# Kernel optimization log

Hardware: AMD Instinct MI355X
Metric: run time of the kernel (lower is better)

## Reference

```python
import jax, jax.numpy as jnp
import numpy as np

B, T, E = 2, 2048, 2048
H = 16
DH = E // H  # 128
FFN = 4 * E  # 8192
EPS = 1e-5


def _layernorm(x, g, b):
    mu = jnp.mean(x, axis=-1, keepdims=True)
    var = jnp.mean((x - mu) ** 2, axis=-1, keepdims=True)
    return (x - mu) * jax.lax.rsqrt(var + EPS) * g + b


def setup_inputs() -> dict:
    key = jax.random.key(0)
    ks = jax.random.split(key, 8)
    s = 0.02
    return {
        "x": jax.random.normal(ks[0], (B, T, E), jnp.float32),
        "g1": jnp.ones((E,), jnp.float32),
        "b1": jnp.zeros((E,), jnp.float32),
        "wq": jax.random.normal(ks[1], (E, E), jnp.float32) * s,
        "wk": jax.random.normal(ks[2], (E, E), jnp.float32) * s,
        "wv": jax.random.normal(ks[3], (E, E), jnp.float32) * s,
        "wo": jax.random.normal(ks[4], (E, E), jnp.float32) * s,
        "g2": jnp.ones((E,), jnp.float32),
        "b2": jnp.zeros((E,), jnp.float32),
        "w1": jax.random.normal(ks[5], (E, FFN), jnp.float32) * s,
        "w2": jax.random.normal(ks[6], (E, FFN), jnp.float32) * s,
        "w3": jax.random.normal(ks[7], (FFN, E), jnp.float32) * s,
    }


def reference(x, g1, b1, wq, wk, wv, wo, g2, b2, w1, w2, w3):
    Bx, Tx, Ex = x.shape
    # --- attention block (pre-LN, residual) ---
    h = _layernorm(x, g1, b1)
    q = (h @ wq).reshape(Bx, Tx, H, DH)
    k = (h @ wk).reshape(Bx, Tx, H, DH)
    v = (h @ wv).reshape(Bx, Tx, H, DH)
    scores = jnp.einsum('bqhd,bkhd->bhqk', q, k) / jnp.sqrt(jnp.float32(DH))
    causal = jnp.tril(jnp.ones((Tx, Tx), bool))  # [T,T]
    scores = jnp.where(causal[None, None], scores, -jnp.inf)
    attn = jax.nn.softmax(scores, axis=-1)
    ctx = jnp.einsum('bhqk,bkhd->bqhd', attn, v).reshape(Bx, Tx, H * DH)
    x = x + ctx @ wo
    # --- SwiGLU MLP block (pre-LN, residual) ---
    h = _layernorm(x, g2, b2)
    gated = jax.nn.silu(h @ w1) * (h @ w2)
    return x + gated @ w3
```

## Files before the change

kernel.cpp:

```cpp
#include <hip/hip_runtime.h>


#define T_SEQ 2048
#define E_DIM 2048
#define N_HEAD 16
#define D_HEAD 128
#define FFN_DIM 8192
#define M_ROWS 4096
#define QS (3 * E_DIM)

typedef unsigned short u16;
typedef short short8 __attribute__((ext_vector_type(8)));
typedef float f32x4 __attribute__((ext_vector_type(4)));

#define DEV __device__ __forceinline__

DEV u16 f2bf(float f) {
  unsigned u = __float_as_uint(f);
  u += 0x7fffu + ((u >> 16) & 1u);
  return (u16)(u >> 16);
}
DEV float bf2f(u16 h) { return __uint_as_float(((unsigned)h) << 16); }

DEV void async16(void* lds, const void* g) {
  __builtin_amdgcn_global_load_lds((const __attribute__((address_space(1))) void*)g,
                                   (__attribute__((address_space(3))) void*)lds, 16, 0, 0);
}

__global__ __launch_bounds__(256) void ln_kernel(const float* __restrict__ x,
                                                 const float* __restrict__ gw,
                                                 const float* __restrict__ bw,
                                                 u16* __restrict__ out) {
  int row = blockIdx.x;
  int t = threadIdx.x;
  const float4* xr = (const float4*)(x + (size_t)row * E_DIM);
  float4 a = xr[t], c = xr[t + 256];
  float s = a.x + a.y + a.z + a.w + c.x + c.y + c.z + c.w;
  float q = a.x * a.x + a.y * a.y + a.z * a.z + a.w * a.w +
            c.x * c.x + c.y * c.y + c.z * c.z + c.w * c.w;
  for (int off = 32; off > 0; off >>= 1) {
    s += __shfl_down(s, off);
    q += __shfl_down(q, off);
  }
  __shared__ float red[8];
  if ((t & 63) == 0) { red[(t >> 6) * 2] = s; red[(t >> 6) * 2 + 1] = q; }
  __syncthreads();
  s = red[0] + red[2] + red[4] + red[6];
  q = red[1] + red[3] + red[5] + red[7];
  float mu = s * (1.f / E_DIM);
  float rs = rsqrtf(q * (1.f / E_DIM) - mu * mu + 1e-5f);
  const float4* g4 = (const float4*)gw;
  const float4* b4 = (const float4*)bw;
  float4 g0 = g4[t], g1v = g4[t + 256], e0 = b4[t], e1 = b4[t + 256];
  ushort4 o0, o1;
  o0.x = f2bf((a.x - mu) * rs * g0.x + e0.x);
  o0.y = f2bf((a.y - mu) * rs * g0.y + e0.y);
  o0.z = f2bf((a.z - mu) * rs * g0.z + e0.z);
  o0.w = f2bf((a.w - mu) * rs * g0.w + e0.w);
  o1.x = f2bf((c.x - mu) * rs * g1v.x + e1.x);
  o1.y = f2bf((c.y - mu) * rs * g1v.y + e1.y);
  o1.z = f2bf((c.z - mu) * rs * g1v.z + e1.z);
  o1.w = f2bf((c.w - mu) * rs * g1v.w + e1.w);
  ((ushort4*)(out + (size_t)row * E_DIM))[t] = o0;
  ((ushort4*)(out + (size_t)row * E_DIM))[t + 256] = o1;
}

__global__ __launch_bounds__(256) void cvt_t_kernel(const float* __restrict__ W,
                                                    u16* __restrict__ WT,
                                                    int Kd, int Nd) {
  __shared__ float tile[32][33];
  int tx = threadIdx.x, ty = threadIdx.y;
  int n0 = blockIdx.x * 32, k0 = blockIdx.y * 32;
#pragma unroll
  for (int i = 0; i < 4; i++)
    tile[ty + i * 8][tx] = W[(size_t)(k0 + ty + i * 8) * Nd + n0 + tx];
  __syncthreads();
#pragma unroll
  for (int i = 0; i < 4; i++)
    WT[(size_t)(n0 + ty + i * 8) * Kd + k0 + tx] = f2bf(tile[tx][ty + i * 8]);
}

__global__ __launch_bounds__(256) void transpose_v_kernel(const u16* __restrict__ qkv,
                                                          u16* __restrict__ vt) {
  __shared__ u16 tile[32][33];
  int tx = threadIdx.x, ty = threadIdx.y;
  int b = blockIdx.z;
  int t0 = blockIdx.x * 32, e0 = blockIdx.y * 32;
#pragma unroll
  for (int i = 0; i < 4; i++)
    tile[ty + i * 8][tx] =
        qkv[(size_t)(b * T_SEQ + t0 + ty + i * 8) * QS + 2 * E_DIM + e0 + tx];
  __syncthreads();
#pragma unroll
  for (int i = 0; i < 4; i++)
    vt[((size_t)b * E_DIM + e0 + ty + i * 8) * T_SEQ + t0 + tx] = tile[tx][ty + i * 8];
}

__global__ __launch_bounds__(256) void add3_kernel(float* __restrict__ out,
                                                   const u16* __restrict__ pk) {
  const size_t MN = (size_t)M_ROWS * E_DIM;
  size_t base = ((size_t)blockIdx.x * 256 + threadIdx.x) * 8;
  short8 a = *(const short8*)(pk + base);
  short8 b = *(const short8*)(pk + MN + base);
  float4 o0 = *(float4*)(out + base), o1 = *(float4*)(out + base + 4);
  o0.x += bf2f((u16)a[0]) + bf2f((u16)b[0]);
  o0.y += bf2f((u16)a[1]) + bf2f((u16)b[1]);
  o0.z += bf2f((u16)a[2]) + bf2f((u16)b[2]);
  o0.w += bf2f((u16)a[3]) + bf2f((u16)b[3]);
  o1.x += bf2f((u16)a[4]) + bf2f((u16)b[4]);
  o1.y += bf2f((u16)a[5]) + bf2f((u16)b[5]);
  o1.z += bf2f((u16)a[6]) + bf2f((u16)b[6]);
  o1.w += bf2f((u16)a[7]) + bf2f((u16)b[7]);
  *(float4*)(out + base) = o0;
  *(float4*)(out + base + 4) = o1;
}

template <int MODE, int BM_>
__global__ __launch_bounds__(512, 1) void gemm8p(const u16* __restrict__ A,
                                                 const u16* __restrict__ BT,
                                                 void* __restrict__ Cout,
                                                 const void* __restrict__ Extra,
                                                 int N, int K, int lda, int ldb,
                                                 int CX, int CY) {
  constexpr int MM = BM_ / 64;
  constexpr int AUNIT = BM_ * 32;
  __shared__ u16 Abuf[4 * AUNIT];
  __shared__ u16 Bbuf[4 * 8192];
  const int t = threadIdx.x;
  const int w = t >> 6, l = t & 63, g = l >> 4, lq = l & 15;
  const int wm = w >> 2, wn = w & 3;

  const int bid = (blockIdx.z * gridDim.y + blockIdx.y) * gridDim.x + blockIdx.x;
  const int xcd = bid & 7, slot = bid >> 3;
  const int nchx = gridDim.x / CX;
  const int nchy = gridDim.y / CY;
  const int cpz = nchx * nchy;
  const int kz = xcd / cpz;
  const int cid = xcd % cpz;
  const int bx = (cid % nchx) * CX + (slot % CX);
  const int by = (cid / nchx) * CY + (slot / CX);
  const size_t bm = (size_t)by * BM_, bn = (size_t)bx * 256;
  const size_t koff = (size_t)kz * K;

  const int srcrow = ((l >> 3) << 1) | (l & 1);
  const int csrc = ((((l >> 1) & 3) ^ ((l >> 3) & 3)) << 3);
  const u16* aSrc = A + (bm + w * 16 + srcrow) * (size_t)lda + koff + csrc;
  const u16* bSrc = BT + (bn + w * 16 + srcrow) * (size_t)ldb + koff + csrc;
  const int rdoff = (((lq & 1) + 2 * (g ^ ((lq >> 1) & 3))) << 3);

#define STA8(DB, KS, TILE)                                                    \
  {                                                                           \
    u16* Ad = Abuf + (DB) * (2 * AUNIT) + (KS)*AUNIT + w * 512;               \
    const u16* as_ = aSrc + (size_t)(TILE)*64 + (KS)*32;                      \
    async16(Ad, as_);                                                         \
    if constexpr (BM_ == 256) async16(Ad + 4096, as_ + (size_t)128 * lda);    \
  }
#define STB8(DB, KS, TILE)                                                    \
  {                                                                           \
    u16* Bd = Bbuf + (DB)*16384 + (KS)*8192 + w * 512;                        \
    const u16* bs_ = bSrc + (size_t)(TILE)*64 + (KS)*32;                      \
    async16(Bd, bs_);                                                         \
    async16(Bd + 4096, bs_ + (size_t)128 * ldb);                              \
  }
#define RDA8(DB, KS, MH)                                                      \
  _Pragma("unroll") for (int mm = 0; mm < MM; ++mm)                           \
      af[mm] = *(const short8*)(Abuf + (DB) * (2 * AUNIT) + (KS)*AUNIT +      \
                                (wm * (BM_ / 4) + (MH) * (BM_ / 8) + mm * 8 + \
                                 (lq >> 1)) * 64 + rdoff);
#define RDB8(DB, KS)                                                          \
  _Pragma("unroll") for (int nn = 0; nn < 4; ++nn)                            \
      bf[nn] = *(const short8*)(Bbuf + (DB)*16384 + (KS)*8192 +               \
                                (wn * 32 + nn * 8 + (lq >> 1)) * 64 + rdoff);
#define MM168(MH)                                                             \
  _Pragma("unroll") for (int mm = 0; mm < MM; ++mm)                           \
      _Pragma("unroll") for (int nn = 0; nn < 4; ++nn)                        \
          acc[(MH)*MM + mm][nn] = __builtin_amdgcn_mfma_f32_16x16x32_bf16(    \
              af[mm], bf[nn], acc[(MH)*MM + mm][nn], 0, 0, 0);
#define SYNCA                                                                 \
  __builtin_amdgcn_s_barrier();                                               \
  asm volatile("s_waitcnt lgkmcnt(0)" ::: "memory");                          \
  __builtin_amdgcn_sched_barrier(0);                                          \
  __builtin_amdgcn_s_setprio(1);
#define ENDP __builtin_amdgcn_s_setprio(0);
#define BAR2 __builtin_amdgcn_s_barrier();
#define WAITN                                                                 \
  if constexpr (BM_ == 256) asm volatile("s_waitcnt vmcnt(8)" ::: "memory");  \
  else                      asm volatile("s_waitcnt vmcnt(6)" ::: "memory");
#define WAITH                                                                 \
  if constexpr (BM_ == 256) asm volatile("s_waitcnt vmcnt(4)" ::: "memory");  \
  else                      asm volatile("s_waitcnt vmcnt(3)" ::: "memory");

  const int NT = K >> 6, NI = NT >> 1;
  f32x4 acc[2 * MM][4] = {};
  short8 af[MM > 4 ? MM : 4], bf[4];

  STA8(0, 0, 0); STB8(0, 0, 0);
  STA8(0, 1, 0); STB8(0, 1, 0);
  STA8(1, 0, 1); STB8(1, 0, 1);
  WAITN;
  BAR2;

  for (int j = 0; j < NI; ++j) {
    const int t1 = 2 * j + 1, t2 = 2 * j + 2, t3 = 2 * j + 3;
    const bool s2 = t2 < NT, s3 = t3 < NT, lastI = (j + 1 == NI);
    RDB8(0, 0); RDA8(0, 0, 0);
    STA8(1, 1, t1);
    SYNCA; MM168(0); ENDP; BAR2;
    RDA8(0, 0, 1);
    STB8(1, 1, t1);
    SYNCA; MM168(1); ENDP;
    WAITN;
    BAR2;
    RDB8(0, 1); RDA8(0, 1, 0);
    if (s2) STA8(0, 0, t2);
    SYNCA; MM168(0); ENDP; BAR2;
    RDA8(0, 1, 1);
    if (s2) STB8(0, 0, t2);
    SYNCA; MM168(1); ENDP;
    if (lastI) { WAITH; } else { WAITN; }
    BAR2;
    RDB8(1, 0); RDA8(1, 0, 0);
    if (s2) STA8(0, 1, t2);
    SYNCA; MM168(0); ENDP; BAR2;
    RDA8(1, 0, 1);
    if (s2) STB8(0, 1, t2);
    SYNCA; MM168(1); ENDP;
    if (lastI) { asm volatile("s_waitcnt vmcnt(0)" ::: "memory"); } else { WAITN; }
    BAR2;
    RDB8(1, 1); RDA8(1, 1, 0);
    if (s3) STA8(1, 0, t3);
    SYNCA; MM168(0); ENDP; BAR2;
    RDA8(1, 1, 1);
    if (s3) STB8(1, 0, t3);
    SYNCA; MM168(1); ENDP;
    if (!lastI) { WAITN; }
    BAR2;
  }
#undef STA8
#undef STB8
#undef RDA8
#undef RDB8
#undef MM168
#undef SYNCA
#undef ENDP
#undef BAR2
#undef WAITN
#undef WAITH

  const size_t mn = (size_t)gridDim.y * BM_ * (size_t)N;
#pragma unroll
  for (int m = 0; m < 2 * MM; m++) {
    size_t row = bm + wm * (BM_ / 2) + m * 16 + 4 * g;
#pragma unroll
    for (int n = 0; n < 4; n++) {
      size_t col = bn + wn * 64 + n * 16 + lq;
#pragma unroll
      for (int r = 0; r < 4; r++) {
        size_t idx = (row + r) * (size_t)N + col;
        if constexpr (MODE == 0) {
          ((u16*)Cout)[idx] = f2bf(acc[m][n][r]);
        } else if constexpr (MODE == 1) {
          ((float*)Cout)[idx] = ((const float*)Extra)[idx] + acc[m][n][r];
        } else if constexpr (MODE == 2) {
          float a = bf2f(((const u16*)Extra)[idx]);
          float sil = a / (1.f + exp2f(-1.4426950408889634f * a));
          ((u16*)Cout)[idx] = f2bf(sil * acc[m][n][r]);
        } else {
          ((u16*)Cout)[(size_t)kz * mn + idx] = f2bf(acc[m][n][r]);
        }
      }
    }
  }
}

__global__ __launch_bounds__(256, 2) void attn_kernel(const u16* __restrict__ QKV,
                                                      const u16* __restrict__ VT,
                                                      u16* __restrict__ CTX) {
  __shared__ u16 Ks[64 * 128];
  __shared__ u16 Vs[128 * 64];
  __shared__ u16 P_all[4][32 * 72];
  const int t = threadIdx.x;
  const int w = t >> 6, l = t & 63, g = l >> 4, lq = l & 15;
  u16* P = P_all[w];
  const int q0blk = blockIdx.x * 128;
  const int q0w = q0blk + w * 32;
  const int bh = blockIdx.y, b = bh >> 4, h = bh & 15;
  const u16* qp = QKV + (size_t)b * T_SEQ * QS + h * D_HEAD;
  const u16* kp = QKV + (size_t)b * T_SEQ * QS + E_DIM + h * D_HEAD;
  const u16* vp = VT + ((size_t)b * E_DIM + h * D_HEAD) * T_SEQ;

  short8 qf[2][4];
#pragma unroll
  for (int rg = 0; rg < 2; rg++)
#pragma unroll
    for (int ks = 0; ks < 4; ks++)
      qf[rg][ks] =
          *(const short8*)(qp + (size_t)(q0w + rg * 16 + lq) * QS + ks * 32 + g * 8);

  f32x4 acc[2][8] = {};
  float m2[2][4], ls[2][4];
#pragma unroll
  for (int rg = 0; rg < 2; rg++)
#pragma unroll
    for (int r = 0; r < 4; r++) { m2[rg][r] = -1e30f; ls[rg][r] = 0.f; }
  const float sc = 0.08838834764831845f * 1.4426950408889634f;

  const int kRow0 = 16 * w + (l >> 4);
  const int kChunk = l & 15;
  const int vRow0 = 32 * w + (l >> 3);
  const int vChunk = l & 7;

  for (int kv0 = 0; kv0 < q0blk + 128; kv0 += 64) {
#pragma unroll
    for (int j = 0; j < 4; j++) {
      int R = kRow0 + 4 * j;
      async16(Ks + (16 * w + 4 * j) * 128,
              kp + (size_t)(kv0 + R) * QS + ((kChunk ^ (R & 7)) << 3));
    }
#pragma unroll
    for (int j = 0; j < 4; j++) {
      int D = vRow0 + 8 * j;
      async16(Vs + (32 * w + 8 * j) * 64,
              vp + (size_t)D * T_SEQ + kv0 + ((vChunk ^ (D & 7)) << 3));
    }
    __syncthreads();

#pragma unroll
    for (int rg = 0; rg < 2; rg++) {
      const int rb = q0w + rg * 16;
      if (kv0 > rb + 15) continue;
      f32x4 s[4];
      __builtin_amdgcn_s_setprio(1);
#pragma unroll
      for (int ct = 0; ct < 4; ct++) {
        s[ct] = f32x4{0.f, 0.f, 0.f, 0.f};
#pragma unroll
        for (int ks = 0; ks < 4; ks++) {
          short8 kf = *(const short8*)(Ks + (ct * 16 + lq) * 128 +
                                       (((ks * 4 + g) ^ (lq & 7)) << 3));
          s[ct] = __builtin_amdgcn_mfma_f32_16x16x32_bf16(qf[rg][ks], kf, s[ct], 0, 0, 0);
        }
      }
      __builtin_amdgcn_s_setprio(0);
      float sv[4][4];
#pragma unroll
      for (int ct = 0; ct < 4; ct++)
#pragma unroll
        for (int r = 0; r < 4; r++) sv[ct][r] = s[ct][r] * sc;
      if (kv0 + 64 > rb) {
#pragma unroll
        for (int ct = 0; ct < 4; ct++)
#pragma unroll
          for (int r = 0; r < 4; r++)
            if (kv0 + ct * 16 + lq > rb + 4 * g + r) sv[ct][r] = -1e30f;
      }
      float mx[4];
#pragma unroll
      for (int r = 0; r < 4; r++)
        mx[r] = fmaxf(fmaxf(sv[0][r], sv[1][r]), fmaxf(sv[2][r], sv[3][r]));
#pragma unroll
      for (int off = 1; off < 16; off <<= 1)
#pragma unroll
        for (int r = 0; r < 4; r++) mx[r] = fmaxf(mx[r], __shfl_xor(mx[r], off));
#pragma unroll
      for (int r = 0; r < 4; r++) {
        float mn = fmaxf(m2[rg][r], mx[r]);
        float sca = exp2f(m2[rg][r] - mn);
        m2[rg][r] = mn;
        float sum = 0.f;
#pragma unroll
        for (int ct = 0; ct < 4; ct++) {
          float pv = exp2f(sv[ct][r] - mn);
          sum += pv;
          P[(rg * 16 + 4 * g + r) * 72 + ct * 16 + lq] = f2bf(pv);
        }
        ls[rg][r] = ls[rg][r] * sca + sum;
#pragma unroll
        for (int n = 0; n < 8; n++) acc[rg][n][r] *= sca;
      }
      short8 pa[2];
#pragma unroll
      for (int ks2 = 0; ks2 < 2; ks2++)
        pa[ks2] = *(const short8*)(P + (rg * 16 + lq) * 72 + ks2 * 32 + g * 8);
      __builtin_amdgcn_s_setprio(1);
#pragma unroll
      for (int n = 0; n < 8; n++)
#pragma unroll
        for (int ks2 = 0; ks2 < 2; ks2++) {
          short8 vf = *(const short8*)(Vs + (n * 16 + lq) * 64 +
                                       (((ks2 * 4 + g) ^ (lq & 7)) << 3));
          acc[rg][n] = __builtin_amdgcn_mfma_f32_16x16x32_bf16(pa[ks2], vf, acc[rg][n], 0, 0, 0);
        }
      __builtin_amdgcn_s_setprio(0);
    }
    __syncthreads();
  }

#pragma unroll
  for (int rg = 0; rg < 2; rg++) {
#pragma unroll
    for (int off = 1; off < 16; off <<= 1)
#pragma unroll
      for (int r = 0; r < 4; r++) ls[rg][r] += __shfl_xor(ls[rg][r], off);
  }
  u16* cp = CTX + ((size_t)b * T_SEQ + q0w) * E_DIM + h * D_HEAD;
#pragma unroll
  for (int rg = 0; rg < 2; rg++) {
    float inv[4];
#pragma unroll
    for (int r = 0; r < 4; r++) inv[r] = 1.f / ls[rg][r];
#pragma unroll
    for (int n = 0; n < 8; n++)
#pragma unroll
      for (int r = 0; r < 4; r++)
        cp[(size_t)(rg * 16 + 4 * g + r) * E_DIM + n * 16 + lq] =
            f2bf(acc[rg][n][r] * inv[r]);
  }
}

extern "C" void kernel_launch(void* const* d_in, const int* in_sizes, int n_in,
                              void* d_out, int out_size, void* d_ws, size_t ws_size,
                              hipStream_t stream) {
  (void)in_sizes; (void)n_in; (void)out_size; (void)ws_size;
  const float* x  = (const float*)d_in[0];
  const float* g1 = (const float*)d_in[1];
  const float* b1 = (const float*)d_in[2];
  const float* wq = (const float*)d_in[3];
  const float* wk = (const float*)d_in[4];
  const float* wv = (const float*)d_in[5];
  const float* wo = (const float*)d_in[6];
  const float* g2 = (const float*)d_in[7];
  const float* b2 = (const float*)d_in[8];
  const float* w1 = (const float*)d_in[9];
  const float* w2 = (const float*)d_in[10];
  const float* w3 = (const float*)d_in[11];
  float* out = (float*)d_out;

  const size_t EE2 = (size_t)E_DIM * E_DIM * 2;
  const size_t EF2 = (size_t)E_DIM * FFN_DIM * 2;
  const size_t ME2 = (size_t)M_ROWS * E_DIM * 2;
  char* p = (char*)d_ws;
  u16* wqkvT = (u16*)p; p += 3 * EE2;
  u16* woT = (u16*)p; p += EE2;
  u16* w1T = (u16*)p; p += EF2;
  u16* w2T = (u16*)p; p += EF2;
  u16* w3T = (u16*)p; p += EF2;
  u16* Hb  = (u16*)p; p += ME2;
  u16* QKVb = (u16*)p; p += (size_t)M_ROWS * QS * 2;
  u16* VTb = (u16*)p; p += ME2;
  u16* CTXb = (u16*)p; p += ME2;
  u16* U1b = QKVb;
  u16* Pk = wqkvT;

  dim3 blk32(32, 8);
  cvt_t_kernel<<<dim3(E_DIM / 32, E_DIM / 32), blk32, 0, stream>>>(wq, wqkvT, E_DIM, E_DIM);
  cvt_t_kernel<<<dim3(E_DIM / 32, E_DIM / 32), blk32, 0, stream>>>(wk, wqkvT + E_DIM * E_DIM, E_DIM, E_DIM);
  cvt_t_kernel<<<dim3(E_DIM / 32, E_DIM / 32), blk32, 0, stream>>>(wv, wqkvT + 2 * E_DIM * E_DIM, E_DIM, E_DIM);
  cvt_t_kernel<<<dim3(E_DIM / 32, E_DIM / 32), blk32, 0, stream>>>(wo, woT, E_DIM, E_DIM);
  cvt_t_kernel<<<dim3(FFN_DIM / 32, E_DIM / 32), blk32, 0, stream>>>(w1, w1T, E_DIM, FFN_DIM);
  cvt_t_kernel<<<dim3(FFN_DIM / 32, E_DIM / 32), blk32, 0, stream>>>(w2, w2T, E_DIM, FFN_DIM);
  cvt_t_kernel<<<dim3(E_DIM / 32, FFN_DIM / 32), blk32, 0, stream>>>(w3, w3T, FFN_DIM, E_DIM);

  ln_kernel<<<M_ROWS, 256, 0, stream>>>(x, g1, b1, Hb);
  gemm8p<0, 256><<<dim3(QS / 256, M_ROWS / 256), 512, 0, stream>>>(
      Hb, wqkvT, QKVb, nullptr, QS, E_DIM, E_DIM, E_DIM, 6, 8);
  transpose_v_kernel<<<dim3(T_SEQ / 32, E_DIM / 32, 2), blk32, 0, stream>>>(QKVb, VTb);
  attn_kernel<<<dim3(T_SEQ / 128, 2 * N_HEAD), 256, 0, stream>>>(QKVb, VTb, CTXb);
  gemm8p<1, 128><<<dim3(E_DIM / 256, M_ROWS / 128), 512, 0, stream>>>(
      CTXb, woT, out, x, E_DIM, E_DIM, E_DIM, E_DIM, 4, 8);

  ln_kernel<<<M_ROWS, 256, 0, stream>>>(out, g2, b2, Hb);
  gemm8p<0, 256><<<dim3(FFN_DIM / 256, M_ROWS / 256), 512, 0, stream>>>(
      Hb, w1T, U1b, nullptr, FFN_DIM, E_DIM, E_DIM, E_DIM, 8, 8);
  gemm8p<2, 256><<<dim3(FFN_DIM / 256, M_ROWS / 256), 512, 0, stream>>>(
      Hb, w2T, U1b, U1b, FFN_DIM, E_DIM, E_DIM, E_DIM, 8, 8);
  gemm8p<3, 256><<<dim3(E_DIM / 256, M_ROWS / 256, 2), 512, 0, stream>>>(
      U1b, w3T, Pk, nullptr, E_DIM, FFN_DIM / 2, FFN_DIM, FFN_DIM, 4, 8);
  add3_kernel<<<4096, 256, 0, stream>>>(out, Pk);
}
```

Before: 893.3 us.

## Fuse W1 and W2 FFN GEMMs into one dual-B kernel with SiLU epilogue

Replaces the two separate FFN up-projection GEMMs (one writing U1 in bf16, the second reading it back to apply SiLU gating) with a single kernel. Each block loads one A tile and matching 128-column tiles of both w1T and w2T. The two products are combined through LDS in the epilogue, so the silu(u1)*u2 result is written once. This removes one full pass over A and the bf16 round trip of the intermediate U1 buffer. In exchange each block covers a narrower 128-column N tile, adds an LDS exchange step in the epilogue, and keeps the pipelined async-load schedule intact.

```diff
diff --git a/kernel.cpp b/kernel.cpp
--- a/kernel.cpp
+++ b/kernel.cpp
@@ -273,6 +273,166 @@
   }
 }
 
+__global__ __launch_bounds__(512, 1) void gemm_ffn(const u16* __restrict__ A,
+                                                   const u16* __restrict__ B1T,
+                                                   const u16* __restrict__ B2T,
+                                                   u16* __restrict__ Cout,
+                                                   int N, int K, int lda, int ldb,
+                                                   int CX, int CY) {
+  constexpr int AUNIT = 8192;
+  __shared__ u16 Abuf[4 * AUNIT];
+  __shared__ u16 Bbuf[4 * AUNIT];
+  const int t = threadIdx.x;
+  const int w = t >> 6, l = t & 63, g = l >> 4, lq = l & 15;
+  const int wm = w >> 2, wn = w & 3;
+
+  const int bid = blockIdx.y * gridDim.x + blockIdx.x;
+  const int xcd = bid & 7, slot = bid >> 3;
+  const int nchx = gridDim.x / CX;
+  const int cid = xcd;
+  const int bx = (cid % nchx) * CX + (slot % CX);
+  const int by = (cid / nchx) * CY + (slot / CX);
+  const size_t bm = (size_t)by * 256;
+  const size_t c0 = (size_t)bx * 128;
+
+  const int srcrow = ((l >> 3) << 1) | (l & 1);
+  const int csrc = ((((l >> 1) & 3) ^ ((l >> 3) & 3)) << 3);
+  const u16* aSrc = A + (bm + w * 16 + srcrow) * (size_t)lda + csrc;
+  const u16* b1Src = B1T + (c0 + w * 16 + srcrow) * (size_t)ldb + csrc;
+  const u16* b2Src = B2T + (c0 + w * 16 + srcrow) * (size_t)ldb + csrc;
+  const int rdoff = (((lq & 1) + 2 * (g ^ ((lq >> 1) & 3))) << 3);
+
+#define STA8(DB, KS, TILE)                                                    \
+  {                                                                           \
+    u16* Ad = Abuf + (DB) * (2 * AUNIT) + (KS)*AUNIT + w * 512;               \
+    const u16* as_ = aSrc + (size_t)(TILE)*64 + (KS)*32;                      \
+    async16(Ad, as_);                                                         \
+    async16(Ad + 4096, as_ + (size_t)128 * lda);                              \
+  }
+#define STB8(DB, KS, TILE)                                                    \
+  {                                                                           \
+    u16* Bd = Bbuf + (DB) * (2 * AUNIT) + (KS)*AUNIT + w * 512;               \
+    size_t off_ = (size_t)(TILE)*64 + (KS)*32;                                \
+    async16(Bd, b1Src + off_);                                                \
+    async16(Bd + 4096, b2Src + off_);                                         \
+  }
+#define RDA8(DB, KS, MH)                                                      \
+  _Pragma("unroll") for (int mm = 0; mm < 4; ++mm)                            \
+      af[mm] = *(const short8*)(Abuf + (DB) * (2 * AUNIT) + (KS)*AUNIT +      \
+                                (wm * 64 + (MH)*32 + mm * 8 + (lq >> 1)) *    \
+                                    64 + rdoff);
+#define RDB8(DB, KS)                                                          \
+  _Pragma("unroll") for (int nn = 0; nn < 4; ++nn)                            \
+      bf[nn] = *(const short8*)(Bbuf + (DB) * (2 * AUNIT) + (KS)*AUNIT +      \
+                                (wn * 32 + nn * 8 + (lq >> 1)) * 64 + rdoff);
+#define MM168(MH)                                                             \
+  _Pragma("unroll") for (int mm = 0; mm < 4; ++mm)                            \
+      _Pragma("unroll") for (int nn = 0; nn < 4; ++nn)                        \
+          acc[(MH)*4 + mm][nn] = __builtin_amdgcn_mfma_f32_16x16x32_bf16(     \
+              af[mm], bf[nn], acc[(MH)*4 + mm][nn], 0, 0, 0);
+#define SYNCA                                                                 \
+  __builtin_amdgcn_s_barrier();                                               \
+  asm volatile("s_waitcnt lgkmcnt(0)" ::: "memory");                          \
+  __builtin_amdgcn_sched_barrier(0);                                          \
+  __builtin_amdgcn_s_setprio(1);
+#define ENDP __builtin_amdgcn_s_setprio(0);
+#define BAR2 __builtin_amdgcn_s_barrier();
+#define WAITN asm volatile("s_waitcnt vmcnt(8)" ::: "memory");
+#define WAITH asm volatile("s_waitcnt vmcnt(4)" ::: "memory");
+
+  const int NT = K >> 6, NI = NT >> 1;
+  f32x4 acc[8][4] = {};
+  short8 af[4], bf[4];
+
+  STA8(0, 0, 0); STB8(0, 0, 0);
+  STA8(0, 1, 0); STB8(0, 1, 0);
+  STA8(1, 0, 1); STB8(1, 0, 1);
+  WAITN;
+  BAR2;
+
+  for (int j = 0; j < NI; ++j) {
+    const int t1 = 2 * j + 1, t2 = 2 * j + 2, t3 = 2 * j + 3;
+    const bool s2 = t2 < NT, s3 = t3 < NT, lastI = (j + 1 == NI);
+    RDB8(0, 0); RDA8(0, 0, 0);
+    STA8(1, 1, t1);
+    SYNCA; MM168(0); ENDP; BAR2;
+    RDA8(0, 0, 1);
+    STB8(1, 1, t1);
+    SYNCA; MM168(1); ENDP;
+    WAITN;
+    BAR2;
+    RDB8(0, 1); RDA8(0, 1, 0);
+    if (s2) STA8(0, 0, t2);
+    SYNCA; MM168(0); ENDP; BAR2;
+    RDA8(0, 1, 1);
+    if (s2) STB8(0, 0, t2);
+    SYNCA; MM168(1); ENDP;
+    if (lastI) { WAITH; } else { WAITN; }
+    BAR2;
+    RDB8(1, 0); RDA8(1, 0, 0);
+    if (s2) STA8(0, 1, t2);
+    SYNCA; MM168(0); ENDP; BAR2;
+    RDA8(1, 0, 1);
+    if (s2) STB8(0, 1, t2);
+    SYNCA; MM168(1); ENDP;
+    if (lastI) { asm volatile("s_waitcnt vmcnt(0)" ::: "memory"); } else { WAITN; }
+    BAR2;
+    RDB8(1, 1); RDA8(1, 1, 0);
+    if (s3) STA8(1, 0, t3);
+    SYNCA; MM168(0); ENDP; BAR2;
+    RDA8(1, 1, 1);
+    if (s3) STB8(1, 0, t3);
+    SYNCA; MM168(1); ENDP;
+    if (!lastI) { WAITN; }
+    BAR2;
+  }
+#undef STA8
+#undef STB8
+#undef RDA8
+#undef RDB8
+#undef MM168
+#undef SYNCA
+#undef ENDP
+#undef BAR2
+#undef WAITN
+#undef WAITH
+
+  const int reg = wm * 2 + ((wn >= 2) ? (wn - 2) : wn);
+  float* fb = (float*)((reg < 2 ? Abuf : Bbuf) + (reg & 1) * 16384);
+  if (wn >= 2) {
+#pragma unroll
+    for (int m = 0; m < 8; m++)
+#pragma unroll
+      for (int n = 0; n < 4; n++)
+#pragma unroll
+        for (int r = 0; r < 4; r++) {
+          int lrow = m * 16 + 4 * g + r;
+          int pcol = (n * 16 + lq) ^ ((g & 1) << 4);
+          fb[lrow * 64 + pcol] = acc[m][n][r];
+        }
+  }
+  __syncthreads();
+  if (wn < 2) {
+#pragma unroll
+    for (int m = 0; m < 8; m++) {
+      size_t row = bm + wm * 128 + m * 16 + 4 * g;
+#pragma unroll
+      for (int n = 0; n < 4; n++) {
+        size_t col = c0 + wn * 64 + n * 16 + lq;
+#pragma unroll
+        for (int r = 0; r < 4; r++) {
+          int lrow = m * 16 + 4 * g + r;
+          int pcol = (n * 16 + lq) ^ ((g & 1) << 4);
+          float u1 = acc[m][n][r];
+          float u2 = fb[lrow * 64 + pcol];
+          float sil = u1 / (1.f + exp2f(-1.4426950408889634f * u1));
+          Cout[(row + r) * (size_t)N + col] = f2bf(sil * u2);
+        }
+      }
+    }
+  }
+}
+
 __global__ __launch_bounds__(256, 2) void attn_kernel(const u16* __restrict__ QKV,
                                                       const u16* __restrict__ VT,
                                                       u16* __restrict__ CTX) {
@@ -470,10 +630,8 @@
       CTXb, woT, out, x, E_DIM, E_DIM, E_DIM, E_DIM, 4, 8);
 
   ln_kernel<<<M_ROWS, 256, 0, stream>>>(out, g2, b2, Hb);
-  gemm8p<0, 256><<<dim3(FFN_DIM / 256, M_ROWS / 256), 512, 0, stream>>>(
-      Hb, w1T, U1b, nullptr, FFN_DIM, E_DIM, E_DIM, E_DIM, 8, 8);
-  gemm8p<2, 256><<<dim3(FFN_DIM / 256, M_ROWS / 256), 512, 0, stream>>>(
-      Hb, w2T, U1b, U1b, FFN_DIM, E_DIM, E_DIM, E_DIM, 8, 8);
+  gemm_ffn<<<dim3(FFN_DIM / 128, M_ROWS / 256), 512, 0, stream>>>(
+      Hb, w1T, w2T, U1b, FFN_DIM, E_DIM, E_DIM, E_DIM, 16, 8);
   gemm8p<3, 256><<<dim3(E_DIM / 256, M_ROWS / 256, 2), 512, 0, stream>>>(
       U1b, w3T, Pk, nullptr, E_DIM, FFN_DIM / 2, FFN_DIM, FFN_DIM, 4, 8);
   add3_kernel<<<4096, 256, 0, stream>>>(out, Pk);
```

Result: no change. 892.3 us (-0.1%).
